# Kernel optimization log

Hardware: AMD Instinct MI355X
Metric: run time of the kernel (lower is better)

The kernel has to match this reference:

```python
import jax, jax.numpy as jnp
import numpy as np

D = 1024
H = 16
HD = D // H
DFF = 4096
NL = 6
CAP = 0.5
EPS = 1e-5


def _layer_norm(x, g, b):
    mu = jnp.mean(x, axis=-1, keepdims=True)
    var = jnp.mean(jnp.square(x - mu), axis=-1, keepdims=True)
    return (x - mu) * jax.lax.rsqrt(var + EPS) * g + b


def _encoder_layer(x, p):
    # p: (Wqkv[3D,D], bqkv[3D], Wo[D,D], bo[D], W1[DFF,D], b1, W2[D,DFF], b2, g1, be1, g2, be2)
    Wqkv, bqkv, Wo, bo, W1, b1, W2, b2, g1, be1, g2, be2 = p
    B, T, _ = x.shape
    qkv = x @ Wqkv.T + bqkv                      # [B,T,3D]
    q, k, v = jnp.split(qkv, 3, axis=-1)
    q = q.reshape(B, T, H, HD)
    k = k.reshape(B, T, H, HD)
    v = v.reshape(B, T, H, HD)
    scores = jnp.einsum('bqhd,bkhd->bhqk', q, k) / jnp.sqrt(jnp.float32(HD))
    attn = jax.nn.softmax(scores, axis=-1)
    o = jnp.einsum('bhqk,bkhd->bqhd', attn, v).reshape(B, T, D)
    o = o @ Wo.T + bo
    x = _layer_norm(x + o, g1, be1)              # post-norm (norm_first=False)
    ff = jax.nn.relu(x @ W1.T + b1) @ W2.T + b2
    x = _layer_norm(x + ff, g2, be2)
    return x


def _mod_route(x, rw, p):
    # rw: [D] router weight; top-k tokens per sequence go through the layer
    B, T, _ = x.shape
    k = max(1, int(T * CAP))
    scores = x @ rw                              # [B,T]
    topk_vals, topk_idx = jax.lax.top_k(scores, k)  # [B,k]
    selected = jnp.take_along_axis(x, topk_idx[:, :, None], axis=1)  # [B,k,D]
    processed = _encoder_layer(selected, p)
    w = jax.nn.sigmoid(topk_vals)[:, :, None]
    delta = (processed - selected) * w
    bidx = jnp.arange(B)[:, None]
    return x.at[bidx, topk_idx].add(delta)


def setup_inputs() -> dict:
    key = jax.random.key(0)
    ks = jax.random.split(key, 16)
    s = 0.02
    inp = {
        'x': jax.random.normal(ks[0], (4, 2048, D), dtype=jnp.float32),
        'Wqkv': jax.random.normal(ks[1], (NL, 3 * D, D), dtype=jnp.float32) * s,
        'bqkv': jnp.zeros((NL, 3 * D), jnp.float32),
        'Wo': jax.random.normal(ks[2], (NL, D, D), dtype=jnp.float32) * s,
        'bo': jnp.zeros((NL, D), jnp.float32),
        'W1': jax.random.normal(ks[3], (NL, DFF, D), dtype=jnp.float32) * s,
        'b1': jnp.zeros((NL, DFF), jnp.float32),
        'W2': jax.random.normal(ks[4], (NL, D, DFF), dtype=jnp.float32) * s,
        'b2': jnp.zeros((NL, D), jnp.float32),
        'ln1g': jnp.ones((NL, D), jnp.float32),
        'ln1b': jnp.zeros((NL, D), jnp.float32),
        'ln2g': jnp.ones((NL, D), jnp.float32),
        'ln2b': jnp.zeros((NL, D), jnp.float32),
        'router_w': jax.random.normal(ks[5], (NL, D), dtype=jnp.float32) * s,
    }
    return inp


def reference(x, Wqkv, bqkv, Wo, bo, W1, b1, W2, b2, ln1g, ln1b, ln2g, ln2b, router_w):
    for i in range(NL):
        p = (Wqkv[i], bqkv[i], Wo[i], bo[i], W1[i], b1[i], W2[i], b2[i],
             ln1g[i], ln1b[i], ln2g[i], ln2b[i])
        if i % 2 == 1:  # mod_every_n=2 -> MoD on odd layers
            x = _mod_route(x, router_w[i], p)
        else:
            x = _encoder_layer(x, p)
    return x
```

## Files before the change

kernel.cpp:

```cpp
#include <hip/hip_runtime.h>
#include <cstdint>
#include <cstddef>


#define DEV_INLINE __device__ __forceinline__

typedef _Float16 half_t;
typedef half_t half8 __attribute__((ext_vector_type(8)));
typedef float f32x4 __attribute__((ext_vector_type(4)));

DEV_INLINE f32x4 mfma16(half8 a, half8 b, f32x4 c) {
    return __builtin_amdgcn_mfma_f32_16x16x32_f16(a, b, c, 0, 0, 0);
}

DEV_INLINE void cvt8(const float4& a, const float4& b, half8& h) {
    h[0] = (half_t)a.x; h[1] = (half_t)a.y; h[2] = (half_t)a.z; h[3] = (half_t)a.w;
    h[4] = (half_t)b.x; h[5] = (half_t)b.y; h[6] = (half_t)b.z; h[7] = (half_t)b.w;
}

__global__ __launch_bounds__(256) void cvt_half8_kernel(
    const float* __restrict__ in, half_t* __restrict__ out, int n8) {
    int i = blockIdx.x * 256 + threadIdx.x;
    if (i >= n8) return;
    const float4* s = (const float4*)in + (size_t)i * 2;
    float4 a = s[0], b = s[1];
    half8 h;
    cvt8(a, b, h);
    ((half8*)out)[i] = h;
}

template <typename AT, typename OT, bool RELU>
__global__ __launch_bounds__(256)
void gemm_bt(const AT* __restrict__ A, const half_t* __restrict__ Bw,
             const float* __restrict__ bias, OT* __restrict__ C,
             int M, int N, int K) {
    constexpr int LP = 40;
    __shared__ half_t As[128 * LP];
    __shared__ half_t Bs[128 * LP];
    const int tid  = threadIdx.x;
    const int bm = blockIdx.x, bn = blockIdx.y;
    const int lane = tid & 63;
    const int wave = tid >> 6;
    const int wm = (wave >> 1) * 64;
    const int wn = (wave & 1) * 64;
    const int lr = lane & 15;
    const int lq = lane >> 4;
    const int lk = lq * 8;

    const int sr = tid >> 1;
    const int sc = (tid & 1) * 16;
    const AT*     aglb = A  + (size_t)(bm * 128 + sr) * K + sc;
    const half_t* bglb = Bw + (size_t)(bn * 128 + sr) * K + sc;
    half_t* adst = &As[sr * LP + sc];
    half_t* bdst = &Bs[sr * LP + sc];

    f32x4 acc[4][4] = {};

    for (int k0 = 0; k0 < K; k0 += 32) {
        __syncthreads();
        if constexpr (sizeof(AT) == 4) {
            const float4* s = (const float4*)(aglb + k0);
            float4 v0 = s[0], v1 = s[1], v2 = s[2], v3 = s[3];
            half8 h0, h1;
            cvt8(v0, v1, h0);
            cvt8(v2, v3, h1);
            *(half8*)adst = h0;
            *(half8*)(adst + 8) = h1;
        } else {
            const half8* s = (const half8*)(aglb + k0);
            half8 v0 = s[0], v1 = s[1];
            *(half8*)adst = v0;
            *(half8*)(adst + 8) = v1;
        }
        {
            const half8* s = (const half8*)(bglb + k0);
            half8 v0 = s[0], v1 = s[1];
            *(half8*)bdst = v0;
            *(half8*)(bdst + 8) = v1;
        }
        __syncthreads();
        half8 af[4], bf[4];
#pragma unroll
        for (int i = 0; i < 4; i++)
            af[i] = *(const half8*)&As[(wm + i * 16 + lr) * LP + lk];
#pragma unroll
        for (int j = 0; j < 4; j++)
            bf[j] = *(const half8*)&Bs[(wn + j * 16 + lr) * LP + lk];
#pragma unroll
        for (int i = 0; i < 4; i++)
#pragma unroll
            for (int j = 0; j < 4; j++)
                acc[i][j] = mfma16(af[i], bf[j], acc[i][j]);
    }

#pragma unroll
    for (int i = 0; i < 4; i++) {
#pragma unroll
        for (int j = 0; j < 4; j++) {
            const int col = bn * 128 + wn + j * 16 + lr;
            const float bv = bias[col];
#pragma unroll
            for (int r = 0; r < 4; r++) {
                const int row = bm * 128 + wm + i * 16 + lq * 4 + r;
                float v = acc[i][j][r] + bv;
                if constexpr (RELU) v = fmaxf(v, 0.0f);
                C[(size_t)row * N + col] = (OT)v;
            }
        }
    }
}

__global__ __launch_bounds__(256)
void attn_kernel(const half_t* __restrict__ qkv, half_t* __restrict__ o, int T) {
    const int qb = blockIdx.x;
    const int b  = blockIdx.y >> 4;
    const int h  = blockIdx.y & 15;
    const int tid = threadIdx.x;
    const int wave = tid >> 6, lane = tid & 63;
    const int lr = lane & 15, lq = lane >> 4, lk = lq * 8;

    __shared__ half_t Qs[64][72];
    __shared__ half_t Ks[64][72];
    __shared__ half_t VT[64][72];
    __shared__ half_t Ps[64][72];
    __shared__ float  Ss[64][65];
    __shared__ float  m_sh[64], l_sh[64], al_sh[64];

    const half_t* base = qkv + (size_t)(b * T) * 3072 + h * 64;

    {
        const int r = tid >> 2, c = (tid & 3) * 16;
        const half_t* src = base + (size_t)(qb * 64 + r) * 3072 + c;
        *(half8*)&Qs[r][c]     = *(const half8*)src;
        *(half8*)&Qs[r][c + 8] = *(const half8*)(src + 8);
    }
    if (tid < 64) { m_sh[tid] = -1e30f; l_sh[tid] = 0.0f; }

    f32x4 oacc[4] = {};

    const int nkb = T >> 6;
    for (int kb = 0; kb < nkb; kb++) {
        __syncthreads();
        {
            const int r = tid >> 2, c = (tid & 3) * 16;
            const half_t* ks = base + 1024 + (size_t)(kb * 64 + r) * 3072 + c;
            *(half8*)&Ks[r][c]     = *(const half8*)ks;
            *(half8*)&Ks[r][c + 8] = *(const half8*)(ks + 8);
            const half_t* vs = base + 2048 + (size_t)(kb * 64 + r) * 3072 + c;
            half8 v0 = *(const half8*)vs;
            half8 v1 = *(const half8*)(vs + 8);
#pragma unroll
            for (int i = 0; i < 8; i++) VT[c + i][r] = v0[i];
#pragma unroll
            for (int i = 0; i < 8; i++) VT[c + 8 + i][r] = v1[i];
        }
        __syncthreads();
        f32x4 sacc[4] = {};
#pragma unroll
        for (int kt = 0; kt < 2; kt++) {
            half8 aq = *(const half8*)&Qs[wave * 16 + lr][kt * 32 + lk];
#pragma unroll
            for (int j = 0; j < 4; j++) {
                half8 bk = *(const half8*)&Ks[j * 16 + lr][kt * 32 + lk];
                sacc[j] = mfma16(aq, bk, sacc[j]);
            }
        }
#pragma unroll
        for (int j = 0; j < 4; j++)
#pragma unroll
            for (int r = 0; r < 4; r++)
                Ss[wave * 16 + lq * 4 + r][j * 16 + lr] = sacc[j][r] * 0.125f;
        __syncthreads();
        if (tid < 64) {
            const int row = tid;
            const float m_old = m_sh[row];
            float mx = m_old;
            for (int c = 0; c < 64; c++) mx = fmaxf(mx, Ss[row][c]);
            const float alpha = __expf(m_old - mx);
            float sum = 0.0f;
            for (int c = 0; c < 64; c++) {
                float pv = __expf(Ss[row][c] - mx);
                sum += pv;
                Ps[row][c] = (half_t)pv;
            }
            m_sh[row] = mx;
            l_sh[row] = l_sh[row] * alpha + sum;
            al_sh[row] = alpha;
        }
        __syncthreads();
        {
            const float a0 = al_sh[wave * 16 + lq * 4 + 0];
            const float a1 = al_sh[wave * 16 + lq * 4 + 1];
            const float a2 = al_sh[wave * 16 + lq * 4 + 2];
            const float a3 = al_sh[wave * 16 + lq * 4 + 3];
#pragma unroll
            for (int j = 0; j < 4; j++) {
                oacc[j][0] *= a0; oacc[j][1] *= a1;
                oacc[j][2] *= a2; oacc[j][3] *= a3;
            }
        }
#pragma unroll
        for (int kt = 0; kt < 2; kt++) {
            half8 ap = *(const half8*)&Ps[wave * 16 + lr][kt * 32 + lk];
#pragma unroll
            for (int j = 0; j < 4; j++) {
                half8 bv = *(const half8*)&VT[j * 16 + lr][kt * 32 + lk];
                oacc[j] = mfma16(ap, bv, oacc[j]);
            }
        }
    }
    half_t* obase = o + (size_t)(b * T + qb * 64) * 1024 + h * 64;
#pragma unroll
    for (int j = 0; j < 4; j++) {
#pragma unroll
        for (int r = 0; r < 4; r++) {
            const int row = wave * 16 + lq * 4 + r;
            float v = oacc[j][r] / l_sh[row];
            obase[(size_t)row * 1024 + j * 16 + lr] = (half_t)v;
        }
    }
}

__global__ __launch_bounds__(256)
void add_ln_kernel(const float* __restrict__ x, const float* __restrict__ r,
                   const float* __restrict__ g, const float* __restrict__ bb,
                   float* __restrict__ out) {
    __shared__ float sh[4];
    const int t = blockIdx.x;
    const int tid = threadIdx.x;
    const float* xr = x + (size_t)t * 1024;
    const float* rr = r + (size_t)t * 1024;
    float v[4];
    float s = 0.0f;
#pragma unroll
    for (int i = 0; i < 4; i++) {
        const int c = tid + i * 256;
        v[i] = xr[c] + rr[c];
        s += v[i];
    }
#pragma unroll
    for (int off = 32; off; off >>= 1) s += __shfl_xor(s, off);
    if ((tid & 63) == 0) sh[tid >> 6] = s;
    __syncthreads();
    const float mean = (sh[0] + sh[1] + sh[2] + sh[3]) * (1.0f / 1024.0f);
    __syncthreads();
    float s2 = 0.0f;
#pragma unroll
    for (int i = 0; i < 4; i++) { const float d = v[i] - mean; s2 += d * d; }
#pragma unroll
    for (int off = 32; off; off >>= 1) s2 += __shfl_xor(s2, off);
    if ((tid & 63) == 0) sh[tid >> 6] = s2;
    __syncthreads();
    const float var = (sh[0] + sh[1] + sh[2] + sh[3]) * (1.0f / 1024.0f);
    const float inv = rsqrtf(var + 1e-5f);
    float* orow = out + (size_t)t * 1024;
#pragma unroll
    for (int i = 0; i < 4; i++) {
        const int c = tid + i * 256;
        orow[c] = (v[i] - mean) * inv * g[c] + bb[c];
    }
}

__global__ __launch_bounds__(256)
void router_scores(const float* __restrict__ x, const float* __restrict__ rw,
                   float* __restrict__ scores, int NT) {
    const int w = blockIdx.x * 4 + (threadIdx.x >> 6);
    const int lane = threadIdx.x & 63;
    if (w >= NT) return;
    const float* xr = x + (size_t)w * 1024;
    float s = 0.0f;
    for (int i = lane; i < 1024; i += 64) s += xr[i] * rw[i];
#pragma unroll
    for (int off = 32; off; off >>= 1) s += __shfl_xor(s, off);
    if (lane == 0) scores[w] = s;
}

__global__ __launch_bounds__(256)
void topk_select(const float* __restrict__ scores, int* __restrict__ idx,
                 float* __restrict__ wsel) {
    __shared__ unsigned keys[2048];
    __shared__ int cnt;
    __shared__ int wsum_gt[4], wsum_eq[4];
    const int b = blockIdx.x;
    const int tid = threadIdx.x;
    const int lane = tid & 63, wv = tid >> 6;
    const float* s = scores + b * 2048;
    for (int t = tid; t < 2048; t += 256) {
        unsigned u = __float_as_uint(s[t]);
        keys[t] = (u & 0x80000000u) ? ~u : (u | 0x80000000u);
    }
    if (tid == 0) cnt = 0;
    __syncthreads();
    unsigned prefix = 0;
    int remaining = 1024;
    for (int bit = 31; bit >= 0; --bit) {
        const unsigned test = (prefix >> bit) | 1u;
        int local = 0;
        for (int t = tid; t < 2048; t += 256)
            if ((keys[t] >> bit) == test) local++;
        atomicAdd(&cnt, local);
        __syncthreads();
        const int c = cnt;
        __syncthreads();
        if (tid == 0) cnt = 0;
        if (c >= remaining) prefix |= (1u << bit);
        else remaining -= c;
        __syncthreads();
    }
    const int base = tid * 8;
    int lgt = 0, leq = 0;
#pragma unroll
    for (int i = 0; i < 8; i++) {
        const unsigned k = keys[base + i];
        lgt += (k > prefix);
        leq += (k == prefix);
    }
    int igt = lgt, ieq = leq;
#pragma unroll
    for (int off = 1; off < 64; off <<= 1) {
        const int ng = __shfl_up(igt, off);
        const int ne = __shfl_up(ieq, off);
        if (lane >= off) { igt += ng; ieq += ne; }
    }
    if (lane == 63) { wsum_gt[wv] = igt; wsum_eq[wv] = ieq; }
    __syncthreads();
    int goff = 0, eoff = 0;
    for (int w = 0; w < wv; w++) { goff += wsum_gt[w]; eoff += wsum_eq[w]; }
    const int n_gt = wsum_gt[0] + wsum_gt[1] + wsum_gt[2] + wsum_gt[3];
    const int need = 1024 - n_gt;
    int pg = goff + igt - lgt;
    int pe = eoff + ieq - leq;
#pragma unroll 1
    for (int i = 0; i < 8; i++) {
        const int t = base + i;
        const unsigned k = keys[t];
        if (k > prefix) {
            idx[b * 1024 + pg] = t;
            wsel[b * 1024 + pg] = 1.0f / (1.0f + __expf(-s[t]));
            pg++;
        } else if (k == prefix) {
            if (pe < need) {
                const int p = n_gt + pe;
                idx[b * 1024 + p] = t;
                wsel[b * 1024 + p] = 1.0f / (1.0f + __expf(-s[t]));
            }
            pe++;
        }
    }
}

__global__ __launch_bounds__(256)
void gather_kernel(const float* __restrict__ x, const int* __restrict__ idx,
                   float* __restrict__ sel) {
    const int j = blockIdx.x;
    const int b = j >> 10;
    const int tok = idx[j];
    const float4* src = (const float4*)(x + (size_t)(b * 2048 + tok) * 1024);
    float4* dst = (float4*)(sel + (size_t)j * 1024);
    dst[threadIdx.x] = src[threadIdx.x];
}

__global__ __launch_bounds__(256)
void scatter_kernel(float* __restrict__ x, const float* __restrict__ sel,
                    const float* __restrict__ proc, const int* __restrict__ idx,
                    const float* __restrict__ w) {
    const int j = blockIdx.x;
    const int b = j >> 10;
    const int tok = idx[j];
    const float wt = w[j];
    float4* dst = (float4*)(x + (size_t)(b * 2048 + tok) * 1024);
    const float4* sp = (const float4*)(sel + (size_t)j * 1024);
    const float4* pp = (const float4*)(proc + (size_t)j * 1024);
    float4 d = dst[threadIdx.x], s = sp[threadIdx.x], p = pp[threadIdx.x];
    d.x += (p.x - s.x) * wt;
    d.y += (p.y - s.y) * wt;
    d.z += (p.z - s.z) * wt;
    d.w += (p.w - s.w) * wt;
    dst[threadIdx.x] = d;
}

struct EncCtx {
    const float *bqkv, *bo, *b1, *b2, *g1, *be1, *g2, *be2;
    const half_t *Wqkv_h, *Wo_h, *W1_h, *W2_h;
    half_t *qkv_h, *o_h, *h_h;
    float *tmp_f, *y_f;
};

static void run_encoder(const EncCtx& c, int layer, const float* xin, float* xout,
                        int N, int T, hipStream_t stream) {
    const half_t* Wq = c.Wqkv_h + (size_t)layer * 3072 * 1024;
    const half_t* Wo = c.Wo_h   + (size_t)layer * 1024 * 1024;
    const half_t* W1 = c.W1_h   + (size_t)layer * 4096 * 1024;
    const half_t* W2 = c.W2_h   + (size_t)layer * 1024 * 4096;
    gemm_bt<float, half_t, false><<<dim3(N / 128, 24), 256, 0, stream>>>(
        xin, Wq, c.bqkv + layer * 3072, c.qkv_h, N, 3072, 1024);
    attn_kernel<<<dim3(T / 64, (N / T) * 16), 256, 0, stream>>>(c.qkv_h, c.o_h, T);
    gemm_bt<half_t, float, false><<<dim3(N / 128, 8), 256, 0, stream>>>(
        c.o_h, Wo, c.bo + layer * 1024, c.tmp_f, N, 1024, 1024);
    add_ln_kernel<<<N, 256, 0, stream>>>(xin, c.tmp_f, c.g1 + layer * 1024,
                                         c.be1 + layer * 1024, c.y_f);
    gemm_bt<float, half_t, true><<<dim3(N / 128, 32), 256, 0, stream>>>(
        c.y_f, W1, c.b1 + layer * 4096, c.h_h, N, 4096, 1024);
    gemm_bt<half_t, float, false><<<dim3(N / 128, 8), 256, 0, stream>>>(
        c.h_h, W2, c.b2 + layer * 1024, c.tmp_f, N, 1024, 4096);
    add_ln_kernel<<<N, 256, 0, stream>>>(c.y_f, c.tmp_f, c.g2 + layer * 1024,
                                         c.be2 + layer * 1024, xout);
}

extern "C" void kernel_launch(void* const* d_in, const int* in_sizes, int n_in,
                              void* d_out, int out_size, void* d_ws, size_t ws_size,
                              hipStream_t stream) {
    (void)in_sizes; (void)n_in; (void)ws_size;
    const float* X    = (const float*)d_in[0];
    const float* Wqkv = (const float*)d_in[1];
    const float* bqkv = (const float*)d_in[2];
    const float* Wo   = (const float*)d_in[3];
    const float* bo   = (const float*)d_in[4];
    const float* W1   = (const float*)d_in[5];
    const float* b1   = (const float*)d_in[6];
    const float* W2   = (const float*)d_in[7];
    const float* b2   = (const float*)d_in[8];
    const float* g1   = (const float*)d_in[9];
    const float* be1  = (const float*)d_in[10];
    const float* g2   = (const float*)d_in[11];
    const float* be2  = (const float*)d_in[12];
    const float* rw   = (const float*)d_in[13];

    float* x = (float*)d_out;
    hipMemcpyAsync(x, X, (size_t)out_size * sizeof(float),
                   hipMemcpyDeviceToDevice, stream);

    char* p = (char*)d_ws;
    auto carve = [&](size_t bytes) -> char* {
        char* r = p;
        p += (bytes + 255) & ~(size_t)255;
        return r;
    };
    const size_t nWqkv = 6ull * 3072 * 1024;
    const size_t nWo   = 6ull * 1024 * 1024;
    const size_t nW1   = 6ull * 4096 * 1024;
    const size_t nW2   = 6ull * 1024 * 4096;
    half_t* Wqkv_h = (half_t*)carve(nWqkv * 2);
    half_t* Wo_h   = (half_t*)carve(nWo * 2);
    half_t* W1_h   = (half_t*)carve(nW1 * 2);
    half_t* W2_h   = (half_t*)carve(nW2 * 2);
    half_t* qkv_h  = (half_t*)carve(8192ull * 3072 * 2);
    half_t* o_h    = (half_t*)carve(8192ull * 1024 * 2);
    half_t* h_h    = (half_t*)carve(8192ull * 4096 * 2);
    float*  tmp_f  = (float*)carve(8192ull * 1024 * 4);
    float*  y_f    = (float*)carve(8192ull * 1024 * 4);
    float*  sel_f  = (float*)carve(4096ull * 1024 * 4);
    float*  proc_f = (float*)carve(4096ull * 1024 * 4);
    float*  scores = (float*)carve(8192ull * 4);
    int*    idx    = (int*)carve(4096ull * 4);
    float*  wsel   = (float*)carve(4096ull * 4);

    auto cvt = [&](const float* src, half_t* dst, size_t n) {
        const int n8 = (int)(n / 8);
        cvt_half8_kernel<<<(n8 + 255) / 256, 256, 0, stream>>>(src, dst, n8);
    };
    cvt(Wqkv, Wqkv_h, nWqkv);
    cvt(Wo, Wo_h, nWo);
    cvt(W1, W1_h, nW1);
    cvt(W2, W2_h, nW2);

    EncCtx c{bqkv, bo, b1, b2, g1, be1, g2, be2,
             Wqkv_h, Wo_h, W1_h, W2_h, qkv_h, o_h, h_h, tmp_f, y_f};

    for (int layer = 0; layer < 6; layer++) {
        if (layer & 1) {
            router_scores<<<2048, 256, 0, stream>>>(x, rw + layer * 1024, scores, 8192);
            topk_select<<<4, 256, 0, stream>>>(scores, idx, wsel);
            gather_kernel<<<4096, 256, 0, stream>>>(x, idx, sel_f);
            run_encoder(c, layer, sel_f, proc_f, 4096, 1024, stream);
            scatter_kernel<<<4096, 256, 0, stream>>>(x, sel_f, proc_f, idx, wsel);
        } else {
            run_encoder(c, layer, x, x, 8192, 2048, stream);
        }
    }
}
```

Baseline: 4.106 ms.

## Use direct global-to-LDS loads, fp16 activation shadows, register softmax, and pre-transposed V

The GEMM now loads fp16 tiles straight into unpadded LDS with global_load_lds and no longer converts fp32 A operands inside the tile loop. To make that possible, add_ln, gather and scatter also write fp16 copies of their outputs. Attention now keeps its online softmax in registers using cross-lane shuffles, which removes the score tile in shared memory and several block barriers. It reads V from a separate transposed buffer built by a new transpose kernel. Buffers are aliased to save workspace, and the unpadded LDS layout may cause bank conflicts.

```diff
diff --git a/kernel.cpp b/kernel.cpp
--- a/kernel.cpp
+++ b/kernel.cpp
@@ -7,6 +7,7 @@
 
 typedef _Float16 half_t;
 typedef half_t half8 __attribute__((ext_vector_type(8)));
+typedef half_t half4 __attribute__((ext_vector_type(4)));
 typedef float f32x4 __attribute__((ext_vector_type(4)));
 
 DEV_INLINE f32x4 mfma16(half8 a, half8 b, f32x4 c) {
@@ -16,6 +17,12 @@
 DEV_INLINE void cvt8(const float4& a, const float4& b, half8& h) {
     h[0] = (half_t)a.x; h[1] = (half_t)a.y; h[2] = (half_t)a.z; h[3] = (half_t)a.w;
     h[4] = (half_t)b.x; h[5] = (half_t)b.y; h[6] = (half_t)b.z; h[7] = (half_t)b.w;
+}
+
+DEV_INLINE void lds_load16(const half_t* g, half_t* l) {
+    __builtin_amdgcn_global_load_lds(
+        (const __attribute__((address_space(1))) void*)g,
+        (__attribute__((address_space(3))) void*)l, 16, 0, 0);
 }
 
 __global__ __launch_bounds__(256) void cvt_half8_kernel(
@@ -29,14 +36,13 @@
     ((half8*)out)[i] = h;
 }
 
-template <typename AT, typename OT, bool RELU>
-__global__ __launch_bounds__(256)
-void gemm_bt(const AT* __restrict__ A, const half_t* __restrict__ Bw,
+template <typename OT, bool RELU>
+__global__ __launch_bounds__(256)
+void gemm_bt(const half_t* __restrict__ A, const half_t* __restrict__ Bw,
              const float* __restrict__ bias, OT* __restrict__ C,
-             int M, int N, int K) {
-    constexpr int LP = 40;
-    __shared__ half_t As[128 * LP];
-    __shared__ half_t Bs[128 * LP];
+             int N, int K) {
+    __shared__ half_t As[128 * 32];
+    __shared__ half_t Bs[128 * 32];
     const int tid  = threadIdx.x;
     const int bm = blockIdx.x, bn = blockIdx.y;
     const int lane = tid & 63;
@@ -47,45 +53,29 @@
     const int lq = lane >> 4;
     const int lk = lq * 8;
 
-    const int sr = tid >> 1;
-    const int sc = (tid & 1) * 16;
-    const AT*     aglb = A  + (size_t)(bm * 128 + sr) * K + sc;
-    const half_t* bglb = Bw + (size_t)(bn * 128 + sr) * K + sc;
-    half_t* adst = &As[sr * LP + sc];
-    half_t* bdst = &Bs[sr * LP + sc];
+    const half_t* aglb = A  + (size_t)(bm * 128 + (tid >> 2)) * K + (tid & 3) * 8;
+    const half_t* bglb = Bw + (size_t)(bn * 128 + (tid >> 2)) * K + (tid & 3) * 8;
+    const size_t rows64 = 64ull * K;
+    const int wbase = __builtin_amdgcn_readfirstlane(tid & 192) * 8;
+    half_t* adst = As + wbase;
+    half_t* bdst = Bs + wbase;
 
     f32x4 acc[4][4] = {};
 
     for (int k0 = 0; k0 < K; k0 += 32) {
         __syncthreads();
-        if constexpr (sizeof(AT) == 4) {
-            const float4* s = (const float4*)(aglb + k0);
-            float4 v0 = s[0], v1 = s[1], v2 = s[2], v3 = s[3];
-            half8 h0, h1;
-            cvt8(v0, v1, h0);
-            cvt8(v2, v3, h1);
-            *(half8*)adst = h0;
-            *(half8*)(adst + 8) = h1;
-        } else {
-            const half8* s = (const half8*)(aglb + k0);
-            half8 v0 = s[0], v1 = s[1];
-            *(half8*)adst = v0;
-            *(half8*)(adst + 8) = v1;
-        }
-        {
-            const half8* s = (const half8*)(bglb + k0);
-            half8 v0 = s[0], v1 = s[1];
-            *(half8*)bdst = v0;
-            *(half8*)(bdst + 8) = v1;
-        }
+        lds_load16(aglb + k0,          adst);
+        lds_load16(aglb + k0 + rows64, adst + 2048);
+        lds_load16(bglb + k0,          bdst);
+        lds_load16(bglb + k0 + rows64, bdst + 2048);
         __syncthreads();
         half8 af[4], bf[4];
 #pragma unroll
         for (int i = 0; i < 4; i++)
-            af[i] = *(const half8*)&As[(wm + i * 16 + lr) * LP + lk];
+            af[i] = *(const half8*)&As[(wm + i * 16 + lr) * 32 + lk];
 #pragma unroll
         for (int j = 0; j < 4; j++)
-            bf[j] = *(const half8*)&Bs[(wn + j * 16 + lr) * LP + lk];
+            bf[j] = *(const half8*)&Bs[(wn + j * 16 + lr) * 32 + lk];
 #pragma unroll
         for (int i = 0; i < 4; i++)
 #pragma unroll
@@ -111,33 +101,55 @@
 }
 
 __global__ __launch_bounds__(256)
-void attn_kernel(const half_t* __restrict__ qkv, half_t* __restrict__ o, int T) {
+void vt_transpose(const half_t* __restrict__ qkv, half_t* __restrict__ vt, int T) {
+    const int tb = blockIdx.x, bh = blockIdx.y;
+    const int b = bh >> 4, h = bh & 15;
+    __shared__ half_t tile[64][72];
+    const int tid = threadIdx.x;
+    const int r = tid >> 2, c = (tid & 3) * 16;
+    const half_t* src = qkv + (size_t)(b * T + tb * 64 + r) * 3072 + 2048 + h * 64 + c;
+    *(half8*)&tile[r][c]     = *(const half8*)src;
+    *(half8*)&tile[r][c + 8] = *(const half8*)(src + 8);
+    __syncthreads();
+    const int d = tid >> 2;
+    half8 o0, o1;
+#pragma unroll
+    for (int i = 0; i < 8; i++) o0[i] = tile[c + i][d];
+#pragma unroll
+    for (int i = 0; i < 8; i++) o1[i] = tile[c + 8 + i][d];
+    half_t* dst = vt + ((size_t)bh * 64 + d) * T + tb * 64 + c;
+    *(half8*)dst = o0;
+    *(half8*)(dst + 8) = o1;
+}
+
+__global__ __launch_bounds__(256)
+void attn_kernel(const half_t* __restrict__ qkv, const half_t* __restrict__ vt,
+                 half_t* __restrict__ o, int T) {
     const int qb = blockIdx.x;
-    const int b  = blockIdx.y >> 4;
-    const int h  = blockIdx.y & 15;
+    const int bh = blockIdx.y;
+    const int b = bh >> 4, h = bh & 15;
     const int tid = threadIdx.x;
     const int wave = tid >> 6, lane = tid & 63;
     const int lr = lane & 15, lq = lane >> 4, lk = lq * 8;
 
     __shared__ half_t Qs[64][72];
     __shared__ half_t Ks[64][72];
-    __shared__ half_t VT[64][72];
+    __shared__ half_t Vs[64][72];
     __shared__ half_t Ps[64][72];
-    __shared__ float  Ss[64][65];
-    __shared__ float  m_sh[64], l_sh[64], al_sh[64];
 
     const half_t* base = qkv + (size_t)(b * T) * 3072 + h * 64;
-
     {
         const int r = tid >> 2, c = (tid & 3) * 16;
         const half_t* src = base + (size_t)(qb * 64 + r) * 3072 + c;
         *(half8*)&Qs[r][c]     = *(const half8*)src;
         *(half8*)&Qs[r][c + 8] = *(const half8*)(src + 8);
     }
-    if (tid < 64) { m_sh[tid] = -1e30f; l_sh[tid] = 0.0f; }
-
+
+    float m_i[4] = {-1e30f, -1e30f, -1e30f, -1e30f};
+    float l_i[4] = {0.f, 0.f, 0.f, 0.f};
     f32x4 oacc[4] = {};
 
+    const half_t* vbase = vt + (size_t)bh * 64 * T;
     const int nkb = T >> 6;
     for (int kb = 0; kb < nkb; kb++) {
         __syncthreads();
@@ -146,13 +158,9 @@
             const half_t* ks = base + 1024 + (size_t)(kb * 64 + r) * 3072 + c;
             *(half8*)&Ks[r][c]     = *(const half8*)ks;
             *(half8*)&Ks[r][c + 8] = *(const half8*)(ks + 8);
-            const half_t* vs = base + 2048 + (size_t)(kb * 64 + r) * 3072 + c;
-            half8 v0 = *(const half8*)vs;
-            half8 v1 = *(const half8*)(vs + 8);
-#pragma unroll
-            for (int i = 0; i < 8; i++) VT[c + i][r] = v0[i];
-#pragma unroll
-            for (int i = 0; i < 8; i++) VT[c + 8 + i][r] = v1[i];
+            const half_t* vs = vbase + (size_t)r * T + kb * 64 + c;
+            *(half8*)&Vs[r][c]     = *(const half8*)vs;
+            *(half8*)&Vs[r][c + 8] = *(const half8*)(vs + 8);
         }
         __syncthreads();
         f32x4 sacc[4] = {};
@@ -168,43 +176,39 @@
 #pragma unroll
         for (int j = 0; j < 4; j++)
 #pragma unroll
-            for (int r = 0; r < 4; r++)
-                Ss[wave * 16 + lq * 4 + r][j * 16 + lr] = sacc[j][r] * 0.125f;
-        __syncthreads();
-        if (tid < 64) {
-            const int row = tid;
-            const float m_old = m_sh[row];
-            float mx = m_old;
-            for (int c = 0; c < 64; c++) mx = fmaxf(mx, Ss[row][c]);
-            const float alpha = __expf(m_old - mx);
+            for (int r = 0; r < 4; r++) sacc[j][r] *= 0.125f;
+        float alpha[4];
+#pragma unroll
+        for (int r = 0; r < 4; r++) {
+            float mx = fmaxf(fmaxf(sacc[0][r], sacc[1][r]),
+                             fmaxf(sacc[2][r], sacc[3][r]));
+#pragma unroll
+            for (int off = 1; off < 16; off <<= 1)
+                mx = fmaxf(mx, __shfl_xor(mx, off));
+            const float mnew = fmaxf(m_i[r], mx);
+            alpha[r] = __expf(m_i[r] - mnew);
+            m_i[r] = mnew;
             float sum = 0.0f;
-            for (int c = 0; c < 64; c++) {
-                float pv = __expf(Ss[row][c] - mx);
+#pragma unroll
+            for (int j = 0; j < 4; j++) {
+                const float pv = __expf(sacc[j][r] - mnew);
                 sum += pv;
-                Ps[row][c] = (half_t)pv;
+                Ps[wave * 16 + lq * 4 + r][j * 16 + lr] = (half_t)pv;
             }
-            m_sh[row] = mx;
-            l_sh[row] = l_sh[row] * alpha + sum;
-            al_sh[row] = alpha;
-        }
-        __syncthreads();
-        {
-            const float a0 = al_sh[wave * 16 + lq * 4 + 0];
-            const float a1 = al_sh[wave * 16 + lq * 4 + 1];
-            const float a2 = al_sh[wave * 16 + lq * 4 + 2];
-            const float a3 = al_sh[wave * 16 + lq * 4 + 3];
-#pragma unroll
-            for (int j = 0; j < 4; j++) {
-                oacc[j][0] *= a0; oacc[j][1] *= a1;
-                oacc[j][2] *= a2; oacc[j][3] *= a3;
-            }
-        }
+#pragma unroll
+            for (int off = 1; off < 16; off <<= 1) sum += __shfl_xor(sum, off);
+            l_i[r] = l_i[r] * alpha[r] + sum;
+        }
+#pragma unroll
+        for (int j = 0; j < 4; j++)
+#pragma unroll
+            for (int r = 0; r < 4; r++) oacc[j][r] *= alpha[r];
 #pragma unroll
         for (int kt = 0; kt < 2; kt++) {
             half8 ap = *(const half8*)&Ps[wave * 16 + lr][kt * 32 + lk];
 #pragma unroll
             for (int j = 0; j < 4; j++) {
-                half8 bv = *(const half8*)&VT[j * 16 + lr][kt * 32 + lk];
+                half8 bv = *(const half8*)&Vs[j * 16 + lr][kt * 32 + lk];
                 oacc[j] = mfma16(ap, bv, oacc[j]);
             }
         }
@@ -215,8 +219,7 @@
 #pragma unroll
         for (int r = 0; r < 4; r++) {
             const int row = wave * 16 + lq * 4 + r;
-            float v = oacc[j][r] / l_sh[row];
-            obase[(size_t)row * 1024 + j * 16 + lr] = (half_t)v;
+            obase[(size_t)row * 1024 + j * 16 + lr] = (half_t)(oacc[j][r] / l_i[r]);
         }
     }
 }
@@ -224,7 +227,7 @@
 __global__ __launch_bounds__(256)
 void add_ln_kernel(const float* __restrict__ x, const float* __restrict__ r,
                    const float* __restrict__ g, const float* __restrict__ bb,
-                   float* __restrict__ out) {
+                   float* __restrict__ out, half_t* __restrict__ out_h) {
     __shared__ float sh[4];
     const int t = blockIdx.x;
     const int tid = threadIdx.x;
@@ -254,10 +257,13 @@
     const float var = (sh[0] + sh[1] + sh[2] + sh[3]) * (1.0f / 1024.0f);
     const float inv = rsqrtf(var + 1e-5f);
     float* orow = out + (size_t)t * 1024;
+    half_t* hrow = out_h + (size_t)t * 1024;
 #pragma unroll
     for (int i = 0; i < 4; i++) {
         const int c = tid + i * 256;
-        orow[c] = (v[i] - mean) * inv * g[c] + bb[c];
+        const float y = (v[i] - mean) * inv * g[c] + bb[c];
+        orow[c] = y;
+        hrow[c] = (half_t)y;
     }
 }
 
@@ -351,17 +357,21 @@
 
 __global__ __launch_bounds__(256)
 void gather_kernel(const float* __restrict__ x, const int* __restrict__ idx,
-                   float* __restrict__ sel) {
+                   float* __restrict__ sel, half_t* __restrict__ sel_h) {
     const int j = blockIdx.x;
     const int b = j >> 10;
     const int tok = idx[j];
     const float4* src = (const float4*)(x + (size_t)(b * 2048 + tok) * 1024);
-    float4* dst = (float4*)(sel + (size_t)j * 1024);
-    dst[threadIdx.x] = src[threadIdx.x];
-}
-
-__global__ __launch_bounds__(256)
-void scatter_kernel(float* __restrict__ x, const float* __restrict__ sel,
+    float4 v = src[threadIdx.x];
+    ((float4*)(sel + (size_t)j * 1024))[threadIdx.x] = v;
+    half4 hv; hv[0] = (half_t)v.x; hv[1] = (half_t)v.y;
+    hv[2] = (half_t)v.z; hv[3] = (half_t)v.w;
+    ((half4*)(sel_h + (size_t)j * 1024))[threadIdx.x] = hv;
+}
+
+__global__ __launch_bounds__(256)
+void scatter_kernel(float* __restrict__ x, half_t* __restrict__ x_h,
+                    const float* __restrict__ sel,
                     const float* __restrict__ proc, const int* __restrict__ idx,
                     const float* __restrict__ w) {
     const int j = blockIdx.x;
@@ -377,34 +387,41 @@
     d.z += (p.z - s.z) * wt;
     d.w += (p.w - s.w) * wt;
     dst[threadIdx.x] = d;
+    half4 hv; hv[0] = (half_t)d.x; hv[1] = (half_t)d.y;
+    hv[2] = (half_t)d.z; hv[3] = (half_t)d.w;
+    ((half4*)(x_h + (size_t)(b * 2048 + tok) * 1024))[threadIdx.x] = hv;
 }
 
 struct EncCtx {
     const float *bqkv, *bo, *b1, *b2, *g1, *be1, *g2, *be2;
     const half_t *Wqkv_h, *Wo_h, *W1_h, *W2_h;
-    half_t *qkv_h, *o_h, *h_h;
+    half_t *qkv_h, *o_h, *h_h, *vt, *y_h;
     float *tmp_f, *y_f;
 };
 
-static void run_encoder(const EncCtx& c, int layer, const float* xin, float* xout,
+static void run_encoder(const EncCtx& c, int layer,
+                        const float* xin, const half_t* xin_h,
+                        float* xout, half_t* xout_h,
                         int N, int T, hipStream_t stream) {
     const half_t* Wq = c.Wqkv_h + (size_t)layer * 3072 * 1024;
     const half_t* Wo = c.Wo_h   + (size_t)layer * 1024 * 1024;
     const half_t* W1 = c.W1_h   + (size_t)layer * 4096 * 1024;
     const half_t* W2 = c.W2_h   + (size_t)layer * 1024 * 4096;
-    gemm_bt<float, half_t, false><<<dim3(N / 128, 24), 256, 0, stream>>>(
-        xin, Wq, c.bqkv + layer * 3072, c.qkv_h, N, 3072, 1024);
-    attn_kernel<<<dim3(T / 64, (N / T) * 16), 256, 0, stream>>>(c.qkv_h, c.o_h, T);
-    gemm_bt<half_t, float, false><<<dim3(N / 128, 8), 256, 0, stream>>>(
-        c.o_h, Wo, c.bo + layer * 1024, c.tmp_f, N, 1024, 1024);
+    const int BH = (N / T) * 16;
+    gemm_bt<half_t, false><<<dim3(N / 128, 24), 256, 0, stream>>>(
+        xin_h, Wq, c.bqkv + layer * 3072, c.qkv_h, 3072, 1024);
+    vt_transpose<<<dim3(T / 64, BH), 256, 0, stream>>>(c.qkv_h, c.vt, T);
+    attn_kernel<<<dim3(T / 64, BH), 256, 0, stream>>>(c.qkv_h, c.vt, c.o_h, T);
+    gemm_bt<float, false><<<dim3(N / 128, 8), 256, 0, stream>>>(
+        c.o_h, Wo, c.bo + layer * 1024, c.tmp_f, 1024, 1024);
     add_ln_kernel<<<N, 256, 0, stream>>>(xin, c.tmp_f, c.g1 + layer * 1024,
-                                         c.be1 + layer * 1024, c.y_f);
-    gemm_bt<float, half_t, true><<<dim3(N / 128, 32), 256, 0, stream>>>(
-        c.y_f, W1, c.b1 + layer * 4096, c.h_h, N, 4096, 1024);
-    gemm_bt<half_t, float, false><<<dim3(N / 128, 8), 256, 0, stream>>>(
-        c.h_h, W2, c.b2 + layer * 1024, c.tmp_f, N, 1024, 4096);
+                                         c.be1 + layer * 1024, c.y_f, c.y_h);
+    gemm_bt<half_t, true><<<dim3(N / 128, 32), 256, 0, stream>>>(
+        c.y_h, W1, c.b1 + layer * 4096, c.h_h, 4096, 1024);
+    gemm_bt<float, false><<<dim3(N / 128, 8), 256, 0, stream>>>(
+        c.h_h, W2, c.b2 + layer * 1024, c.tmp_f, 1024, 4096);
     add_ln_kernel<<<N, 256, 0, stream>>>(c.y_f, c.tmp_f, c.g2 + layer * 1024,
-                                         c.be2 + layer * 1024, xout);
+                                         c.be2 + layer * 1024, xout, xout_h);
 }
 
 extern "C" void kernel_launch(void* const* d_in, const int* in_sizes, int n_in,
@@ -444,9 +461,15 @@
     half_t* Wo_h   = (half_t*)carve(nWo * 2);
     half_t* W1_h   = (half_t*)carve(nW1 * 2);
     half_t* W2_h   = (half_t*)carve(nW2 * 2);
-    half_t* qkv_h  = (half_t*)carve(8192ull * 3072 * 2);
-    half_t* o_h    = (half_t*)carve(8192ull * 1024 * 2);
-    half_t* h_h    = (half_t*)carve(8192ull * 4096 * 2);
+    half_t* big0   = (half_t*)carve(8192ull * 4096 * 2);
+    half_t* qkv_h  = big0;
+    half_t* vt     = big0 + 8192ull * 3072;
+    half_t* h_h    = big0;
+    half_t* big1   = (half_t*)carve(8192ull * 1024 * 2);
+    half_t* o_h    = big1;
+    half_t* y_h    = big1;
+    half_t* x_h    = (half_t*)carve(8192ull * 1024 * 2);
+    half_t* sel_h  = (half_t*)carve(4096ull * 1024 * 2);
     float*  tmp_f  = (float*)carve(8192ull * 1024 * 4);
     float*  y_f    = (float*)carve(8192ull * 1024 * 4);
     float*  sel_f  = (float*)carve(4096ull * 1024 * 4);
@@ -463,19 +486,20 @@
     cvt(Wo, Wo_h, nWo);
     cvt(W1, W1_h, nW1);
     cvt(W2, W2_h, nW2);
+    cvt(X, x_h, 8192ull * 1024);
 
     EncCtx c{bqkv, bo, b1, b2, g1, be1, g2, be2,
-             Wqkv_h, Wo_h, W1_h, W2_h, qkv_h, o_h, h_h, tmp_f, y_f};
+             Wqkv_h, Wo_h, W1_h, W2_h, qkv_h, o_h, h_h, vt, y_h, tmp_f, y_f};
 
     for (int layer = 0; layer < 6; layer++) {
         if (layer & 1) {
             router_scores<<<2048, 256, 0, stream>>>(x, rw + layer * 1024, scores, 8192);
             topk_select<<<4, 256, 0, stream>>>(scores, idx, wsel);
-            gather_kernel<<<4096, 256, 0, stream>>>(x, idx, sel_f);
-            run_encoder(c, layer, sel_f, proc_f, 4096, 1024, stream);
-            scatter_kernel<<<4096, 256, 0, stream>>>(x, sel_f, proc_f, idx, wsel);
+            gather_kernel<<<4096, 256, 0, stream>>>(x, idx, sel_f, sel_h);
+            run_encoder(c, layer, sel_f, sel_h, proc_f, y_h, 4096, 1024, stream);
+            scatter_kernel<<<4096, 256, 0, stream>>>(x, x_h, sel_f, proc_f, idx, wsel);
         } else {
-            run_encoder(c, layer, x, x, 8192, 2048, stream);
-        }
-    }
-}
+            run_encoder(c, layer, x, x_h, x, x_h, 8192, 2048, stream);
+        }
+    }
+}
```

New measurement: 3.428 ms. -16.5%, faster.
